# Performance work log

Hardware: AMD Instinct MI355X
Metric: run time of the kernel (lower is better)

## Reference

```python
import jax, jax.numpy as jnp
import numpy as np


def _conv2d(x, w, pad):
    return jax.lax.conv_general_dilated(
        x, w, (1, 1), [(pad, pad), (pad, pad)],
        dimension_numbers=('NCHW', 'OIHW', 'NCHW'))


def _affine_grid(theta, k):
    # torch F.affine_grid, align_corners=False; output size (k, k)
    base = ((2.0 * jnp.arange(k) + 1.0) / k - 1.0).astype(jnp.float32)
    pts = jnp.stack([
        jnp.broadcast_to(base[None, :], (k, k)),  # x varies along width
        jnp.broadcast_to(base[:, None], (k, k)),  # y varies along height
        jnp.ones((k, k), jnp.float32)], -1)        # [k,k,3]
    return jnp.einsum('ijc,nrc->nijr', pts, theta)  # [N,k,k,2] -> (x,y)


def _grid_sample(img, grid):
    # torch F.grid_sample: bilinear, zeros padding, align_corners=False
    # img [C,H,W], grid [k,k,2] with (x,y) in [-1,1]
    C, H, W = img.shape
    gx = (grid[..., 0] + 1.0) * W * 0.5 - 0.5
    gy = (grid[..., 1] + 1.0) * H * 0.5 - 0.5
    x0 = jnp.floor(gx); y0 = jnp.floor(gy)
    wx = gx - x0; wy = gy - y0
    x0i = x0.astype(jnp.int32); y0i = y0.astype(jnp.int32)

    def gath(yi, xi):
        valid = ((xi >= 0) & (xi < W) & (yi >= 0) & (yi < H)).astype(img.dtype)
        v = img[:, jnp.clip(yi, 0, H - 1), jnp.clip(xi, 0, W - 1)]  # [C,k,k]
        return v * valid[None]

    v00 = gath(y0i, x0i); v01 = gath(y0i, x0i + 1)
    v10 = gath(y0i + 1, x0i); v11 = gath(y0i + 1, x0i + 1)
    return (v00 * ((1 - wx) * (1 - wy))[None] + v01 * (wx * (1 - wy))[None]
            + v10 * ((1 - wx) * wy)[None] + v11 * (wx * wy)[None])


def reference(x, stn0_w, stn0_b, stn1_w, lin_w, lin_b, check):
    B, C, H, W = x.shape
    k = stn1_w.shape[-1]
    h = jax.nn.relu(_conv2d(x, stn0_w, k // 2) + stn0_b[None, :, None, None])
    ident6 = jnp.array([1., 0., 0., 0., 1., 0.], jnp.float32)
    out = _conv2d(h, stn1_w, 0) * (1.0 - check) + ident6[None, :, None, None]
    Ho, Wo = out.shape[2], out.shape[3]
    N = B * Ho * Wo
    # permute(0,3,2,1).view(N,2,3) as in torch
    theta = out.transpose(0, 3, 2, 1).reshape(N, 2, 3)
    grid = _affine_grid(theta, k)  # [N,k,k,2]
    xv = jnp.arange(k // 2, k // 2 + Ho, dtype=jnp.float32)[:, None]  # meshgrid 'ij'
    yv = jnp.arange(k // 2, k // 2 + Wo, dtype=jnp.float32)[None, :]
    half = float(k // 2)
    auxx = ((grid[..., 0] * half).reshape(B, Ho, Wo, k, k)
            + xv[None, :, :, None, None]).reshape(N, k, k) / (H - 1) * 2.0 - 1.0
    auxy = ((grid[..., 1] * half).reshape(B, Ho, Wo, k, k)
            + yv[None, :, :, None, None]).reshape(N, k, k) / (W - 1) * 2.0 - 1.0
    auxgrid = jnp.stack([auxx, auxy], -1).reshape(B, Ho * Wo, k, k, 2)
    # tile(x,0,Ho*Wo) duplicates x[b] for each of its Ho*Wo grids; gather directly
    xs = jax.vmap(lambda img, g: jax.vmap(lambda gg: _grid_sample(img, gg))(g))(x, auxgrid)  # [B,P,C,k,k]
    x_out = xs.reshape(N, -1) @ lin_w.T + lin_b  # [N,O]
    score = x_out.reshape(B, Ho, Wo, -1).transpose(0, 3, 2, 1)  # [B,O,Wo,Ho] as in torch
    ident23 = jnp.array([[1., 0., 0.], [0., 1., 0.]], jnp.float32)
    return score, ident23[None] - theta, out, auxx, auxy


def setup_inputs() -> dict:
    key = jax.random.key(0)
    ks = jax.random.split(key, 6)
    C, O, k = 128, 256, 3
    B, H, W = 8, 56, 56
    x = jax.random.normal(ks[0], (B, C, H, W), jnp.float32)
    stn0_w = jax.random.normal(ks[1], (C, C, k, k), jnp.float32) * (1.0 / np.sqrt(C * k * k))
    stn0_b = jax.random.normal(ks[2], (C,), jnp.float32) * 0.01
    # original zero-inits stn1; use small random so theta is non-trivial
    stn1_w = jax.random.normal(ks[3], (6, C, k, k), jnp.float32) * 0.01
    lin_w = jax.random.normal(ks[4], (O, C * k * k), jnp.float32) * (1.0 / np.sqrt(C * k * k))
    lin_b = jax.random.normal(ks[5], (O,), jnp.float32) * 0.01
    return {'x': x, 'stn0_w': stn0_w, 'stn0_b': stn0_b, 'stn1_w': stn1_w,
            'lin_w': lin_w, 'lin_b': lin_b, 'check': 0}
```

## Files before the change

kernel.cpp:

```cpp
#include <hip/hip_runtime.h>

typedef __attribute__((ext_vector_type(4))) float f32x4;
typedef __attribute__((ext_vector_type(8))) short bf16x8;

#define OPLANE 2916
#define NN 23328
#define KDIM 1152
#define PLANE 3136
#define LDP 72

__device__ __forceinline__ unsigned short f2bf(float f) {
    unsigned u = __builtin_bit_cast(unsigned, f);
    u += 0x7fffu + ((u >> 16) & 1u);
    return (unsigned short)(u >> 16);
}
__device__ __forceinline__ float bf2f(unsigned short h) {
    unsigned u = ((unsigned)h) << 16;
    return __builtin_bit_cast(float, u);
}

__global__ __launch_bounds__(256) void k_prep(const float* __restrict__ w0,
                                              const float* __restrict__ lw,
                                              unsigned short* __restrict__ b1t,
                                              unsigned short* __restrict__ b2t) {
    int idx = blockIdx.x * 256 + threadIdx.x;
    if (idx < 147456) {
        int r = idx / KDIM, k = idx - r * KDIM;
        int ij = k >> 7, ic = k & 127;
        b1t[idx] = f2bf(w0[r * KDIM + ic * 9 + ij]);
    } else {
        int j = idx - 147456;
        int r = j / KDIM, k = j - r * KDIM;
        int ij = k >> 7, ic = k & 127;
        b2t[j] = f2bf(lw[r * KDIM + ic * 9 + ij]);
    }
}

__global__ __launch_bounds__(256) void k_nhwc(const float* __restrict__ x,
                                              unsigned short* __restrict__ xnh) {
    __shared__ unsigned short lds[56 * 132];
    const int y = blockIdx.x, b = blockIdx.y, tid = threadIdx.x;
    for (int i = tid; i < 7168; i += 256) {
        int ic = i / 56, xc = i - ic * 56;
        lds[xc * 132 + ic] = f2bf(x[(b * 128 + ic) * PLANE + y * 56 + xc]);
    }
    __syncthreads();
    for (int i = tid; i < 7168; i += 256) {
        int xc = i >> 7, ic = i & 127;
        xnh[(b * PLANE + y * 56 + xc) * 128 + ic] = lds[xc * 132 + ic];
    }
}

__global__ __launch_bounds__(256) void k_gemm1(const unsigned short* __restrict__ xnh,
                                               const unsigned short* __restrict__ Bt,
                                               const float* __restrict__ bias,
                                               float* __restrict__ C) {
    __shared__ unsigned short As[64 * LDP];
    __shared__ unsigned short Bs[64 * LDP];
    const int tid = threadIdx.x;
    const int lane = tid & 63, wid = tid >> 6;
    const int wr = wid >> 1, wc = wid & 1;
    const int n0 = blockIdx.x * 64;
    const int m0 = blockIdx.y * 64;

    f32x4 acc[2][2];
    #pragma unroll
    for (int mt = 0; mt < 2; mt++)
        #pragma unroll
        for (int nt = 0; nt < 2; nt++) { acc[mt][nt][0]=0.f; acc[mt][nt][1]=0.f; acc[mt][nt][2]=0.f; acc[mt][nt][3]=0.f; }

    const int row = tid >> 2, q = tid & 3;
    const int p = m0 + row;
    const int b = p / PLANE; int rem = p - b * PLANE;
    const int y = rem / 56; const int xc = rem - y * 56;
    unsigned short* asw = &As[row * LDP + q * 16];
    const unsigned short* bg = Bt + (n0 + row) * KDIM + q * 16;
    unsigned short* bsw = &Bs[row * LDP + q * 16];
    const int lm = lane & 15, lq = lane >> 4;

    #pragma unroll
    for (int it = 0; it < 18; it++) {
        const int ij = it >> 1;
        const int di = ij / 3, dj = ij - di * 3;
        const int icb = (it & 1) << 6;
        uint4 a0 = make_uint4(0u,0u,0u,0u), a1 = make_uint4(0u,0u,0u,0u);
        bool valid = (y + di >= 1) && (y + di <= 56) && (xc + dj >= 1) && (xc + dj <= 56);
        if (valid) {
            const unsigned short* ap = xnh + (p + (di - 1) * 56 + (dj - 1)) * 128 + icb + q * 16;
            a0 = *(const uint4*)ap;
            a1 = *(const uint4*)(ap + 8);
        }
        uint4 bv0 = *(const uint4*)(bg + it * 64);
        uint4 bv1 = *(const uint4*)(bg + it * 64 + 8);
        __syncthreads();
        *(uint4*)(asw + 0) = a0;  *(uint4*)(asw + 8) = a1;
        *(uint4*)(bsw + 0) = bv0; *(uint4*)(bsw + 8) = bv1;
        __syncthreads();
        #pragma unroll
        for (int kk = 0; kk < 64; kk += 32) {
            bf16x8 af[2], bf[2];
            #pragma unroll
            for (int mt = 0; mt < 2; mt++)
                af[mt] = *(const bf16x8*)&As[(wr * 32 + mt * 16 + lm) * LDP + kk + lq * 8];
            #pragma unroll
            for (int nt = 0; nt < 2; nt++)
                bf[nt] = *(const bf16x8*)&Bs[(wc * 32 + nt * 16 + lm) * LDP + kk + lq * 8];
            #pragma unroll
            for (int mt = 0; mt < 2; mt++)
                #pragma unroll
                for (int nt = 0; nt < 2; nt++)
                    acc[mt][nt] = __builtin_amdgcn_mfma_f32_16x16x32_bf16(af[mt], bf[nt], acc[mt][nt], 0, 0, 0);
        }
    }
    #pragma unroll
    for (int mt = 0; mt < 2; mt++) {
        int m = m0 + wr * 32 + mt * 16 + lq * 4;
        #pragma unroll
        for (int nt = 0; nt < 2; nt++) {
            int n = n0 + wc * 32 + nt * 16 + lm;
            float bb = bias[n];
            #pragma unroll
            for (int r = 0; r < 4; r++)
                C[(m + r) * 128 + n] = fmaxf(acc[mt][nt][r] + bb, 0.f);
        }
    }
}

__global__ __launch_bounds__(256) void k_conv2f(const float* __restrict__ h,
                                                const float* __restrict__ w1,
                                                const int* __restrict__ check,
                                                float* __restrict__ o_out,
                                                float* __restrict__ o_th,
                                                float* __restrict__ o_ax,
                                                float* __restrict__ o_ay,
                                                float* __restrict__ sxy) {
    __shared__ float wlds[6912];
    __shared__ float red[16 * 6 * 17];
    __shared__ float vals[96];
    const int tid = threadIdx.x;
    for (int idx = tid; idx < 6912; idx += 256) {
        int r = idx / KDIM, k = idx - r * KDIM;
        int ij = k >> 7, ic = k & 127;
        wlds[idx] = w1[r * KDIM + ic * 9 + ij];
    }
    __syncthreads();
    const int pt = tid >> 4, c = tid & 15;
    const int p = blockIdx.x * 16 + pt;
    int b = p / OPLANE; int rem = p - b * OPLANE; int oh = rem / 54; int ow = rem - oh * 54;
    const float4* h4 = (const float4*)h;
    const float4* w4 = (const float4*)wlds;
    float acc[6] = {0.f, 0.f, 0.f, 0.f, 0.f, 0.f};
    const int base_sp = b * PLANE + oh * 56 + ow;
    #pragma unroll
    for (int i = 0; i < 3; i++) {
        #pragma unroll
        for (int j = 0; j < 3; j++) {
            int sp = base_sp + i * 56 + j;
            float4 h0 = h4[sp * 32 + c * 2];
            float4 h1 = h4[sp * 32 + c * 2 + 1];
            int ij = i * 3 + j;
            #pragma unroll
            for (int r = 0; r < 6; r++) {
                float4 wa = w4[r * 288 + ij * 32 + c * 2];
                float4 wb = w4[r * 288 + ij * 32 + c * 2 + 1];
                acc[r] += h0.x * wa.x + h0.y * wa.y + h0.z * wa.z + h0.w * wa.w
                        + h1.x * wb.x + h1.y * wb.y + h1.z * wb.z + h1.w * wb.w;
            }
        }
    }
    #pragma unroll
    for (int r = 0; r < 6; r++) red[(pt * 6 + r) * 17 + c] = acc[r];
    __syncthreads();
    if (tid < 96) {
        const float* rp = &red[tid * 17];
        float s = 0.f;
        #pragma unroll
        for (int e = 0; e < 16; e++) s += rp[e];
        vals[tid] = s;
    }
    __syncthreads();
    if (tid < 16) {
        int p2 = blockIdx.x * 16 + tid;
        int b2 = p2 / OPLANE; int r2 = p2 - b2 * OPLANE; int oh2 = r2 / 54; int ow2 = r2 - oh2 * 54;
        float val[6];
        float s = 1.0f - (float)check[0];
        const float id6[6] = {1.f, 0.f, 0.f, 0.f, 1.f, 0.f};
        #pragma unroll
        for (int r = 0; r < 6; r++) val[r] = vals[tid * 6 + r] * s + id6[r];
        int n = (b2 * 54 + ow2) * 54 + oh2;
        #pragma unroll
        for (int r = 0; r < 6; r++) {
            o_out[((b2 * 6 + r) * 54 + oh2) * 54 + ow2] = val[r];
            o_th[n * 6 + r] = id6[r] - val[r];
        }
        const float bse[3] = {-2.f / 3.f, 0.f, 2.f / 3.f};
        #pragma unroll
        for (int i = 0; i < 3; i++)
            #pragma unroll
            for (int j = 0; j < 3; j++) {
                float gx = bse[j] * val[0] + bse[i] * val[1] + val[2];
                float gy = bse[j] * val[3] + bse[i] * val[4] + val[5];
                float ax = (gx + 1.f + (float)ow2) * (2.f / 55.f) - 1.f;
                float ay = (gy + 1.f + (float)oh2) * (2.f / 55.f) - 1.f;
                int ij = i * 3 + j;
                o_ax[n * 9 + ij] = ax;
                o_ay[n * 9 + ij] = ay;
                sxy[(n * 9 + ij) * 2 + 0] = (ax + 1.f) * 28.f - 0.5f;
                sxy[(n * 9 + ij) * 2 + 1] = (ay + 1.f) * 28.f - 0.5f;
            }
    }
}

__global__ __launch_bounds__(256) void k_sgemm(const unsigned short* __restrict__ xnh,
                                               const unsigned short* __restrict__ Wt,
                                               const float* __restrict__ bias,
                                               const float* __restrict__ sxy,
                                               float* __restrict__ score) {
    __shared__ unsigned short Ss[64 * LDP];
    __shared__ unsigned short Ws[128 * LDP];
    const int tid = threadIdx.x;
    const int lane = tid & 63, wid = tid >> 6;
    const int wr = wid >> 1, wc = wid & 1;
    const int o0 = blockIdx.x * 128;
    const int s0 = blockIdx.y * 64;

    f32x4 acc[4][2];
    #pragma unroll
    for (int mt = 0; mt < 4; mt++)
        #pragma unroll
        for (int nt = 0; nt < 2; nt++) { acc[mt][nt][0]=0.f; acc[mt][nt][1]=0.f; acc[mt][nt][2]=0.f; acc[mt][nt][3]=0.f; }

    const int row = tid >> 2, q = tid & 3;
    const int mp = min(s0 + row, NN - 1);
    const int b = mp / OPLANE; const int rr = mp - b * OPLANE;
    const int ho = rr / 54, wo = rr - (rr / 54) * 54;
    const int n = (b * 54 + wo) * 54 + ho;
    const int xbase = b * PLANE;
    unsigned short* ssw = &Ss[row * LDP + q * 16];
    const int wrow = tid >> 1, wq = tid & 1;
    const unsigned short* wg = Wt + (o0 + wrow) * KDIM + wq * 32;
    unsigned short* wsw = &Ws[wrow * LDP + wq * 32];
    const int lm = lane & 15, lq = lane >> 4;

    int off0 = 0, off1 = 0, off2 = 0, off3 = 0;
    float wt0 = 0.f, wt1 = 0.f, wt2 = 0.f, wt3 = 0.f;

    #pragma unroll
    for (int it = 0; it < 18; it++) {
        const int icb = (it & 1) << 6;
        if ((it & 1) == 0) {
            const int ij = it >> 1;
            float sx = sxy[(n * 9 + ij) * 2 + 0];
            float sy = sxy[(n * 9 + ij) * 2 + 1];
            float x0f = floorf(sx), y0f = floorf(sy);
            float wx = sx - x0f, wy = sy - y0f;
            int x0 = (int)x0f, y0 = (int)y0f;
            int x1 = x0 + 1, y1 = y0 + 1;
            float vx0 = (x0 >= 0 && x0 < 56) ? 1.f : 0.f;
            float vx1 = (x1 >= 0 && x1 < 56) ? 1.f : 0.f;
            float vy0 = (y0 >= 0 && y0 < 56) ? 1.f : 0.f;
            float vy1 = (y1 >= 0 && y1 < 56) ? 1.f : 0.f;
            int xc0 = min(max(x0, 0), 55), xc1 = min(max(x1, 0), 55);
            int yc0 = min(max(y0, 0), 55), yc1 = min(max(y1, 0), 55);
            off0 = (xbase + yc0 * 56 + xc0) << 7;
            off1 = (xbase + yc0 * 56 + xc1) << 7;
            off2 = (xbase + yc1 * 56 + xc0) << 7;
            off3 = (xbase + yc1 * 56 + xc1) << 7;
            wt0 = vy0 * vx0 * (1.f - wx) * (1.f - wy);
            wt1 = vy0 * vx1 * wx * (1.f - wy);
            wt2 = vy1 * vx0 * (1.f - wx) * wy;
            wt3 = vy1 * vx1 * wx * wy;
        }
        const int co = icb + q * 16;
        uint4 p0a = *(const uint4*)(xnh + off0 + co);
        uint4 p0b = *(const uint4*)(xnh + off0 + co + 8);
        uint4 p1a = *(const uint4*)(xnh + off1 + co);
        uint4 p1b = *(const uint4*)(xnh + off1 + co + 8);
        uint4 p2a = *(const uint4*)(xnh + off2 + co);
        uint4 p2b = *(const uint4*)(xnh + off2 + co + 8);
        uint4 p3a = *(const uint4*)(xnh + off3 + co);
        uint4 p3b = *(const uint4*)(xnh + off3 + co + 8);
        uint4 w0v = *(const uint4*)(wg + it * 64);
        uint4 w1v = *(const uint4*)(wg + it * 64 + 8);
        uint4 w2v = *(const uint4*)(wg + it * 64 + 16);
        uint4 w3v = *(const uint4*)(wg + it * 64 + 24);
        unsigned dw[8];
        const unsigned* d0 = (const unsigned*)&p0a;
        const unsigned* d1 = (const unsigned*)&p1a;
        const unsigned* d2 = (const unsigned*)&p2a;
        const unsigned* d3 = (const unsigned*)&p3a;
        const unsigned* e0 = (const unsigned*)&p0b;
        const unsigned* e1 = (const unsigned*)&p1b;
        const unsigned* e2 = (const unsigned*)&p2b;
        const unsigned* e3 = (const unsigned*)&p3b;
        #pragma unroll
        for (int d = 0; d < 8; d++) {
            unsigned u0 = (d < 4) ? d0[d] : e0[d - 4];
            unsigned u1 = (d < 4) ? d1[d] : e1[d - 4];
            unsigned u2 = (d < 4) ? d2[d] : e2[d - 4];
            unsigned u3 = (d < 4) ? d3[d] : e3[d - 4];
            float lo = wt0 * __builtin_bit_cast(float, u0 << 16)
                     + wt1 * __builtin_bit_cast(float, u1 << 16)
                     + wt2 * __builtin_bit_cast(float, u2 << 16)
                     + wt3 * __builtin_bit_cast(float, u3 << 16);
            float hi = wt0 * __builtin_bit_cast(float, u0 & 0xffff0000u)
                     + wt1 * __builtin_bit_cast(float, u1 & 0xffff0000u)
                     + wt2 * __builtin_bit_cast(float, u2 & 0xffff0000u)
                     + wt3 * __builtin_bit_cast(float, u3 & 0xffff0000u);
            dw[d] = (unsigned)f2bf(lo) | ((unsigned)f2bf(hi) << 16);
        }
        __syncthreads();
        *(uint4*)(ssw + 0) = *(uint4*)&dw[0];
        *(uint4*)(ssw + 8) = *(uint4*)&dw[4];
        *(uint4*)(wsw + 0)  = w0v;
        *(uint4*)(wsw + 8)  = w1v;
        *(uint4*)(wsw + 16) = w2v;
        *(uint4*)(wsw + 24) = w3v;
        __syncthreads();
        #pragma unroll
        for (int kk = 0; kk < 64; kk += 32) {
            bf16x8 wf[4], sf[2];
            #pragma unroll
            for (int mt = 0; mt < 4; mt++)
                wf[mt] = *(const bf16x8*)&Ws[(wr * 64 + mt * 16 + lm) * LDP + kk + lq * 8];
            #pragma unroll
            for (int nt = 0; nt < 2; nt++)
                sf[nt] = *(const bf16x8*)&Ss[(wc * 32 + nt * 16 + lm) * LDP + kk + lq * 8];
            #pragma unroll
            for (int mt = 0; mt < 4; mt++)
                #pragma unroll
                for (int nt = 0; nt < 2; nt++)
                    acc[mt][nt] = __builtin_amdgcn_mfma_f32_16x16x32_bf16(wf[mt], sf[nt], acc[mt][nt], 0, 0, 0);
        }
    }
    #pragma unroll
    for (int mt = 0; mt < 4; mt++) {
        #pragma unroll
        for (int r = 0; r < 4; r++) {
            int o = o0 + wr * 64 + mt * 16 + lq * 4 + r;
            float bb = bias[o];
            #pragma unroll
            for (int nt = 0; nt < 2; nt++) {
                int s = s0 + wc * 32 + nt * 16 + lm;
                if (s < NN) {
                    int sb = s / OPLANE;
                    int soff = s - sb * OPLANE;
                    score[(sb * 256 + o) * OPLANE + soff] = acc[mt][nt][r] + bb;
                }
            }
        }
    }
}

extern "C" void kernel_launch(void* const* d_in, const int* in_sizes, int n_in,
                              void* d_out, int out_size, void* d_ws, size_t ws_size,
                              hipStream_t stream) {
    const float* x  = (const float*)d_in[0];
    const float* w0 = (const float*)d_in[1];
    const float* b0 = (const float*)d_in[2];
    const float* w1 = (const float*)d_in[3];
    const float* lw = (const float*)d_in[4];
    const float* lb = (const float*)d_in[5];
    const int* check = (const int*)d_in[6];

    float* out   = (float*)d_out;
    float* score = out;
    float* o_th  = out + 5971968;
    float* o_out = out + 6111936;
    float* o_ax  = out + 6251904;
    float* o_ay  = out + 6461856;

    char* wsb = (char*)d_ws;
    float* h   = (float*)wsb;
    unsigned short* xnh = (unsigned short*)(wsb + 12845056);
    unsigned short* b1t = (unsigned short*)(wsb + 19267584);
    unsigned short* b2t = (unsigned short*)(wsb + 19562496);
    float* sxy = (float*)(wsb + 20152320);

    k_prep<<<1728, 256, 0, stream>>>(w0, lw, b1t, b2t);
    k_nhwc<<<dim3(56, 8), 256, 0, stream>>>(x, xnh);
    k_gemm1<<<dim3(2, 392), 256, 0, stream>>>(xnh, b1t, b0, h);
    k_conv2f<<<1458, 256, 0, stream>>>(h, w1, check, o_out, o_th, o_ax, o_ay, sxy);
    k_sgemm<<<dim3(2, 365), 256, 0, stream>>>(xnh, b2t, lb, sxy, score);
}
```

Before: 171.7 us.

## Software-pipeline global loads in conv and grid-sample GEMM loops

Both MFMA main loops now issue the global loads for the next K-step right after the LDS stores and before the current step's MFMA work. This lets memory latency overlap with compute, using register prefetching instead of a double-buffered LDS. The grid-sample kernel also preloads all nine sample coordinates per row up front, rather than reading them inside the loop. The cost is higher register pressure, which could reduce occupancy.

```diff
diff --git a/kernel.cpp b/kernel.cpp
--- a/kernel.cpp
+++ b/kernel.cpp
@@ -78,24 +78,30 @@
     unsigned short* bsw = &Bs[row * LDP + q * 16];
     const int lm = lane & 15, lq = lane >> 4;
 
-    #pragma unroll
-    for (int it = 0; it < 18; it++) {
+    uint4 a0, a1, bv0, bv1;
+    auto issue = [&](int it) {
         const int ij = it >> 1;
         const int di = ij / 3, dj = ij - di * 3;
         const int icb = (it & 1) << 6;
-        uint4 a0 = make_uint4(0u,0u,0u,0u), a1 = make_uint4(0u,0u,0u,0u);
+        a0 = make_uint4(0u,0u,0u,0u); a1 = make_uint4(0u,0u,0u,0u);
         bool valid = (y + di >= 1) && (y + di <= 56) && (xc + dj >= 1) && (xc + dj <= 56);
         if (valid) {
             const unsigned short* ap = xnh + (p + (di - 1) * 56 + (dj - 1)) * 128 + icb + q * 16;
             a0 = *(const uint4*)ap;
             a1 = *(const uint4*)(ap + 8);
         }
-        uint4 bv0 = *(const uint4*)(bg + it * 64);
-        uint4 bv1 = *(const uint4*)(bg + it * 64 + 8);
+        bv0 = *(const uint4*)(bg + it * 64);
+        bv1 = *(const uint4*)(bg + it * 64 + 8);
+    };
+    issue(0);
+
+    #pragma unroll
+    for (int it = 0; it < 18; it++) {
         __syncthreads();
         *(uint4*)(asw + 0) = a0;  *(uint4*)(asw + 8) = a1;
         *(uint4*)(bsw + 0) = bv0; *(uint4*)(bsw + 8) = bv1;
         __syncthreads();
+        if (it < 17) issue(it + 1);
         #pragma unroll
         for (int kk = 0; kk < 64; kk += 32) {
             bf16x8 af[2], bf[2];
@@ -242,48 +248,60 @@
     unsigned short* wsw = &Ws[wrow * LDP + wq * 32];
     const int lm = lane & 15, lq = lane >> 4;
 
+    float2 sc[9];
+    {
+        const float* spp = sxy + n * 18;
+        #pragma unroll
+        for (int ij = 0; ij < 9; ij++) sc[ij] = *(const float2*)(spp + ij * 2);
+    }
+
     int off0 = 0, off1 = 0, off2 = 0, off3 = 0;
     float wt0 = 0.f, wt1 = 0.f, wt2 = 0.f, wt3 = 0.f;
+    auto mkoff = [&](int ij) {
+        float sx = sc[ij].x, sy = sc[ij].y;
+        float x0f = floorf(sx), y0f = floorf(sy);
+        float wx = sx - x0f, wy = sy - y0f;
+        int x0 = (int)x0f, y0 = (int)y0f;
+        int x1 = x0 + 1, y1 = y0 + 1;
+        float vx0 = (x0 >= 0 && x0 < 56) ? 1.f : 0.f;
+        float vx1 = (x1 >= 0 && x1 < 56) ? 1.f : 0.f;
+        float vy0 = (y0 >= 0 && y0 < 56) ? 1.f : 0.f;
+        float vy1 = (y1 >= 0 && y1 < 56) ? 1.f : 0.f;
+        int xc0 = min(max(x0, 0), 55), xc1 = min(max(x1, 0), 55);
+        int yc0 = min(max(y0, 0), 55), yc1 = min(max(y1, 0), 55);
+        off0 = (xbase + yc0 * 56 + xc0) << 7;
+        off1 = (xbase + yc0 * 56 + xc1) << 7;
+        off2 = (xbase + yc1 * 56 + xc0) << 7;
+        off3 = (xbase + yc1 * 56 + xc1) << 7;
+        wt0 = vy0 * vx0 * (1.f - wx) * (1.f - wy);
+        wt1 = vy0 * vx1 * wx * (1.f - wy);
+        wt2 = vy1 * vx0 * (1.f - wx) * wy;
+        wt3 = vy1 * vx1 * wx * wy;
+    };
+
+    uint4 p0a, p0b, p1a, p1b, p2a, p2b, p3a, p3b;
+    uint4 w0v, w1v, w2v, w3v;
+    auto issue = [&](int it) {
+        const int co = ((it & 1) << 6) + q * 16;
+        p0a = *(const uint4*)(xnh + off0 + co);
+        p0b = *(const uint4*)(xnh + off0 + co + 8);
+        p1a = *(const uint4*)(xnh + off1 + co);
+        p1b = *(const uint4*)(xnh + off1 + co + 8);
+        p2a = *(const uint4*)(xnh + off2 + co);
+        p2b = *(const uint4*)(xnh + off2 + co + 8);
+        p3a = *(const uint4*)(xnh + off3 + co);
+        p3b = *(const uint4*)(xnh + off3 + co + 8);
+        w0v = *(const uint4*)(wg + it * 64);
+        w1v = *(const uint4*)(wg + it * 64 + 8);
+        w2v = *(const uint4*)(wg + it * 64 + 16);
+        w3v = *(const uint4*)(wg + it * 64 + 24);
+    };
+
+    mkoff(0);
+    issue(0);
 
     #pragma unroll
     for (int it = 0; it < 18; it++) {
-        const int icb = (it & 1) << 6;
-        if ((it & 1) == 0) {
-            const int ij = it >> 1;
-            float sx = sxy[(n * 9 + ij) * 2 + 0];
-            float sy = sxy[(n * 9 + ij) * 2 + 1];
-            float x0f = floorf(sx), y0f = floorf(sy);
-            float wx = sx - x0f, wy = sy - y0f;
-            int x0 = (int)x0f, y0 = (int)y0f;
-            int x1 = x0 + 1, y1 = y0 + 1;
-            float vx0 = (x0 >= 0 && x0 < 56) ? 1.f : 0.f;
-            float vx1 = (x1 >= 0 && x1 < 56) ? 1.f : 0.f;
-            float vy0 = (y0 >= 0 && y0 < 56) ? 1.f : 0.f;
-            float vy1 = (y1 >= 0 && y1 < 56) ? 1.f : 0.f;
-            int xc0 = min(max(x0, 0), 55), xc1 = min(max(x1, 0), 55);
-            int yc0 = min(max(y0, 0), 55), yc1 = min(max(y1, 0), 55);
-            off0 = (xbase + yc0 * 56 + xc0) << 7;
-            off1 = (xbase + yc0 * 56 + xc1) << 7;
-            off2 = (xbase + yc1 * 56 + xc0) << 7;
-            off3 = (xbase + yc1 * 56 + xc1) << 7;
-            wt0 = vy0 * vx0 * (1.f - wx) * (1.f - wy);
-            wt1 = vy0 * vx1 * wx * (1.f - wy);
-            wt2 = vy1 * vx0 * (1.f - wx) * wy;
-            wt3 = vy1 * vx1 * wx * wy;
-        }
-        const int co = icb + q * 16;
-        uint4 p0a = *(const uint4*)(xnh + off0 + co);
-        uint4 p0b = *(const uint4*)(xnh + off0 + co + 8);
-        uint4 p1a = *(const uint4*)(xnh + off1 + co);
-        uint4 p1b = *(const uint4*)(xnh + off1 + co + 8);
-        uint4 p2a = *(const uint4*)(xnh + off2 + co);
-        uint4 p2b = *(const uint4*)(xnh + off2 + co + 8);
-        uint4 p3a = *(const uint4*)(xnh + off3 + co);
-        uint4 p3b = *(const uint4*)(xnh + off3 + co + 8);
-        uint4 w0v = *(const uint4*)(wg + it * 64);
-        uint4 w1v = *(const uint4*)(wg + it * 64 + 8);
-        uint4 w2v = *(const uint4*)(wg + it * 64 + 16);
-        uint4 w3v = *(const uint4*)(wg + it * 64 + 24);
         unsigned dw[8];
         const unsigned* d0 = (const unsigned*)&p0a;
         const unsigned* d1 = (const unsigned*)&p1a;
@@ -317,6 +335,10 @@
         *(uint4*)(wsw + 16) = w2v;
         *(uint4*)(wsw + 24) = w3v;
         __syncthreads();
+        if (it < 17) {
+            if (((it + 1) & 1) == 0) mkoff((it + 1) >> 1);
+            issue(it + 1);
+        }
         #pragma unroll
         for (int kk = 0; kk < 64; kk += 32) {
             bf16x8 wf[4], sf[2];
```

Measured after the change: 168.9 us. No clear change (-1.6%).
